# Kernel optimization log

Hardware: AMD Instinct MI355X
Metric: run time of the kernel (lower is better)

Reference implementation:

```python
import jax, jax.numpy as jnp
import numpy as np

EMBED_DIM = 64
N_EMBED = 1024
BATCH, H, W = 16, 64, 64


def setup_inputs() -> dict:
    key = jax.random.key(0)
    k1, k2 = jax.random.split(key)
    inputs = jax.random.normal(k1, (BATCH, H, W, EMBED_DIM), dtype=jnp.float32)
    # codebook as in Quantize.build: RandomNormal(stddev=1.0), shape (embed_dim, n_embed)
    cluster_mean = jax.random.normal(k2, (EMBED_DIM, N_EMBED), dtype=jnp.float32)
    return {"inputs": inputs, "cluster_mean": cluster_mean}


def reference(inputs, cluster_mean):
    # inputs: [B,H,W,D]; cluster_mean: [D,K]
    D = cluster_mean.shape[0]
    samples = inputs.reshape(-1, D)  # [N,D]
    dist = (
        jnp.sum(samples * samples, axis=1, keepdims=True)
        - 2.0 * (samples @ cluster_mean)
        + jnp.sum(cluster_mean * cluster_mean, axis=0, keepdims=True)
    )
    cluster_index = jnp.argmin(dist, axis=1).reshape(inputs.shape[:-1])  # [B,H,W]
    quantize = cluster_mean.T[cluster_index]  # gather -> [B,H,W,D]
    q_loss = jnp.mean((quantize - jax.lax.stop_gradient(inputs)) ** 2)
    e_loss = jnp.mean((jax.lax.stop_gradient(quantize) - inputs) ** 2)
    loss = q_loss + 0.25 * e_loss
    # straight-through estimator
    outputs = inputs + jax.lax.stop_gradient(quantize - inputs)
    return outputs, cluster_index, loss
```

## Files before the change

### kernel.cpp

```cpp
#include <hip/hip_runtime.h>
#include <stdint.h>

#define NS 65536
#define D 64
#define K 1024
#define NEL 4194304
#define MARGIN_KEY 0.025f

typedef short bf16x8 __attribute__((ext_vector_type(8)));
typedef short s16x4 __attribute__((ext_vector_type(4)));
typedef float f32x4 __attribute__((ext_vector_type(4)));

static __device__ __forceinline__ unsigned short bf16_rne(float x) {
    union { float f; uint32_t u; } v; v.f = x;
    uint32_t r = v.u + 0x7FFFu + ((v.u >> 16) & 1u);
    return (unsigned short)(r >> 16);
}
static __device__ __forceinline__ float bf16f(unsigned short h) {
    union { uint32_t u; float f; } v; v.u = ((uint32_t)h) << 16;
    return v.f;
}

__global__ __launch_bounds__(256) void vq_prep(
    const float* __restrict__ cm,
    unsigned short* __restrict__ P,
    float* __restrict__ cnorm,
    double* __restrict__ acc)
{
    const int tx = threadIdx.x;
    const int col = tx & 15;
    const int dg = tx >> 4;
    const int b = blockIdx.x;
    const int k = b * 16 + col;
    if (b == 0 && tx == 0) *acc = 0.0;

    float p = 0.f;
    s16x4 hv, lv;
#pragma unroll
    for (int j = 0; j < 4; ++j) {
        float v = cm[(dg * 4 + j) * K + k];
        unsigned short hb = bf16_rne(v);
        hv[j] = (short)hb;
        lv[j] = (short)bf16_rne(v - bf16f(hb));
        p = fmaf(v, v, p);
    }
    const int lane = ((dg >> 1) & 3) * 16 + col;
    const int e0 = (dg & 1) * 4;
    unsigned short* ph = P + ((size_t)(b * 4 + (dg >> 3)) * 64 + lane) * 8 + e0;
    unsigned short* pl = P + ((size_t)(b * 4 + 2 + (dg >> 3)) * 64 + lane) * 8 + e0;
    *(s16x4*)ph = hv;
    *(s16x4*)pl = lv;

    __shared__ float pn[16][17];
    pn[col][dg] = p;
    __syncthreads();
    if (tx < 16) {
        float s = 0.f;
#pragma unroll
        for (int g = 0; g < 16; ++g) s += pn[tx][g];
        cnorm[b * 16 + tx] = s;
    }
}

__global__ __launch_bounds__(256, 2) void vq_main(
    const float* __restrict__ xin,
    const float* __restrict__ cm,
    const unsigned short* __restrict__ P,
    const float* __restrict__ cnorm,
    float* __restrict__ outq,
    float* __restrict__ outidx,
    double* __restrict__ acc_g)
{
    __shared__ char smemA[36864];
    __shared__ unsigned short btile[4][2048];
    __shared__ float cn_lds[1024];
    __shared__ int   widx[128];

    unsigned short* xh = (unsigned short*)smemA;
    unsigned short* xl = (unsigned short*)(smemA + 18432);
    float* mb1 = (float*)smemA;
    float* mb2 = (float*)(smemA + 8704);
    float* red = (float*)smemA;

    const int tx = threadIdx.x;
    const int S0 = blockIdx.x * 128;
    const int w = tx >> 6, l = tx & 63;
    const int quad = l >> 4, col = l & 15;

#define ISSUE(T) do {                                                          \
        const unsigned short* g_ = P + (size_t)(T) * 2048 + tx * 8;            \
        __builtin_amdgcn_global_load_lds(g_, &btile[(T) & 3][tx * 8], 16, 0, 0); \
    } while (0)
#define WAITV(N) asm volatile("s_waitcnt vmcnt(" #N ")" ::: "memory")

    ISSUE(0); ISSUE(1); ISSUE(2);

    {
        const int s = tx >> 2, d0 = (tx & 3) * 16;
#pragma unroll
        for (int half = 0; half < 2; ++half) {
            const int ss = s + half * 64;
            const float* gp = xin + (size_t)(S0 + ss) * D + d0;
            bf16x8 hv0, hv1, lv0, lv1;
#pragma unroll
            for (int j = 0; j < 8; ++j) {
                float va = -gp[j], vb = -gp[8 + j];
                unsigned short ha = bf16_rne(va), hb = bf16_rne(vb);
                hv0[j] = (short)ha; hv1[j] = (short)hb;
                lv0[j] = (short)bf16_rne(va - bf16f(ha));
                lv1[j] = (short)bf16_rne(vb - bf16f(hb));
            }
            *(bf16x8*)(xh + ss * 72 + d0)     = hv0;
            *(bf16x8*)(xh + ss * 72 + d0 + 8) = hv1;
            *(bf16x8*)(xl + ss * 72 + d0)     = lv0;
            *(bf16x8*)(xl + ss * 72 + d0 + 8) = lv1;
        }
#pragma unroll
        for (int q = 0; q < 4; ++q)
            cn_lds[q * 256 + tx] = 0.5f * cnorm[q * 256 + tx];
    }
    __syncthreads();

    bf16x8 AH0[2], AH1[2], AL0[2], AL1[2];
#pragma unroll
    for (int sg = 0; sg < 2; ++sg) {
        const int srow = w * 32 + sg * 16 + col;
        AH0[sg] = *(const bf16x8*)(xh + srow * 72 + quad * 8);
        AH1[sg] = *(const bf16x8*)(xh + srow * 72 + 32 + quad * 8);
        AL0[sg] = *(const bf16x8*)(xl + srow * 72 + quad * 8);
        AL1[sg] = *(const bf16x8*)(xl + srow * 72 + 32 + quad * 8);
    }

    float b1[2][4], b2[2][4];
#pragma unroll
    for (int sg = 0; sg < 2; ++sg)
#pragma unroll
        for (int r = 0; r < 4; ++r) { b1[sg][r] = 3.4e38f; b2[sg][r] = 3.4e38f; }

#define BODY(T) do {                                                           \
        const unsigned short* bt_ = &btile[(T) & 3][0];                        \
        bf16x8 bh0 = *(const bf16x8*)(bt_ + l * 8);                            \
        bf16x8 bh1 = *(const bf16x8*)(bt_ + 512 + l * 8);                      \
        bf16x8 bl0 = *(const bf16x8*)(bt_ + 1024 + l * 8);                     \
        bf16x8 bl1 = *(const bf16x8*)(bt_ + 1536 + l * 8);                     \
        const float cnv_ = cn_lds[(T) * 16 + col];                             \
        const f32x4 cA_ = {cnv_, cnv_, cnv_, cnv_};                            \
        const f32x4 z4_ = {0.f, 0.f, 0.f, 0.f};                                \
        const unsigned tt_ = (unsigned)(T);                                    \
        _Pragma("unroll")                                                      \
        for (int sg = 0; sg < 2; ++sg) {                                       \
            f32x4 a1_ = __builtin_amdgcn_mfma_f32_16x16x32_bf16(AH0[sg], bh0, cA_, 0, 0, 0); \
            a1_ = __builtin_amdgcn_mfma_f32_16x16x32_bf16(AH1[sg], bh1, a1_, 0, 0, 0); \
            a1_ = __builtin_amdgcn_mfma_f32_16x16x32_bf16(AL0[sg], bh0, a1_, 0, 0, 0); \
            f32x4 a2_ = __builtin_amdgcn_mfma_f32_16x16x32_bf16(AH0[sg], bl0, z4_, 0, 0, 0); \
            a2_ = __builtin_amdgcn_mfma_f32_16x16x32_bf16(AH1[sg], bl1, a2_, 0, 0, 0); \
            a2_ = __builtin_amdgcn_mfma_f32_16x16x32_bf16(AL1[sg], bh1, a2_, 0, 0, 0); \
            _Pragma("unroll")                                                  \
            for (int r = 0; r < 4; ++r) {                                      \
                float v_ = a1_[r] + a2_[r];                                    \
                unsigned pu_ = (__builtin_bit_cast(unsigned, v_) & 0xFFFFFFC0u) | tt_; \
                float f_ = __builtin_bit_cast(float, pu_);                     \
                b2[sg][r] = __builtin_amdgcn_fmed3f(b1[sg][r], f_, b2[sg][r]); \
                b1[sg][r] = fminf(b1[sg][r], f_);                              \
            }                                                                  \
        }                                                                      \
    } while (0)

    for (int t = 0; t < 61; ++t) {
        WAITV(2);
        __builtin_amdgcn_s_barrier();
        ISSUE(t + 3);
        BODY(t);
    }
    WAITV(2); __builtin_amdgcn_s_barrier(); BODY(61);
    WAITV(1); __builtin_amdgcn_s_barrier(); BODY(62);
    WAITV(0); __builtin_amdgcn_s_barrier(); BODY(63);

#pragma unroll
    for (int sg = 0; sg < 2; ++sg) {
        const int u = (w * 2 + sg) * 64 + l;
        const int sk = 4 * (u + (u >> 4));
#pragma unroll
        for (int r = 0; r < 4; ++r) {
            mb1[sk + r] = b1[sg][r];
            mb2[sk + r] = b2[sg][r];
        }
    }
    __syncthreads();

    if (tx < 128) {
        const int mw = tx >> 5, msg = (tx >> 4) & 1, mq = (tx >> 2) & 3, mr = tx & 3;
        float B1 = 3.4e38f, B2 = 3.4e38f; int I1 = 0, I2 = 0;
#pragma unroll
        for (int c = 0; c < 16; ++c) {
            const int u = (mw * 2 + msg) * 64 + mq * 16 + c;
            const int e = 4 * (u + (u >> 4)) + mr;
            float v1 = mb1[e];
            float v2 = mb2[e];
            int j1 = (int)(__builtin_bit_cast(unsigned, v1) & 63u) * 16 + c;
            int j2 = (int)(__builtin_bit_cast(unsigned, v2) & 63u) * 16 + c;
            if (v1 < B1)      { B2 = B1; I2 = I1; B1 = v1; I1 = j1; }
            else if (v1 < B2) { B2 = v1; I2 = j1; }
            if (v2 < B1)      { B2 = B1; I2 = I1; B1 = v2; I1 = j2; }
            else if (v2 < B2) { B2 = v2; I2 = j2; }
        }
        int winner = I1;
        if (B2 - B1 < MARGIN_KEY) {
            const float* xp = xin + (size_t)(S0 + tx) * D;
            float a0 = 0, a1 = 0, a2 = 0, a3 = 0, e0 = 0, e1 = 0, e2 = 0, e3 = 0;
            for (int dd = 0; dd < D; dd += 4) {
                float x0 = xp[dd], x1 = xp[dd + 1], x2 = xp[dd + 2], x3 = xp[dd + 3];
                a0 = fmaf(x0, cm[(dd + 0) * K + I1], a0);
                a1 = fmaf(x1, cm[(dd + 1) * K + I1], a1);
                a2 = fmaf(x2, cm[(dd + 2) * K + I1], a2);
                a3 = fmaf(x3, cm[(dd + 3) * K + I1], a3);
                e0 = fmaf(x0, cm[(dd + 0) * K + I2], e0);
                e1 = fmaf(x1, cm[(dd + 1) * K + I2], e1);
                e2 = fmaf(x2, cm[(dd + 2) * K + I2], e2);
                e3 = fmaf(x3, cm[(dd + 3) * K + I2], e3);
            }
            float d1 = cn_lds[I1] - ((a0 + a1) + (a2 + a3));
            float d2 = cn_lds[I2] - ((e0 + e1) + (e2 + e3));
            if (d2 < d1 || (d2 == d1 && I2 < I1)) winner = I2;
        }
        widx[tx] = winner;
    }
    __syncthreads();

    float psum = 0.f;
#pragma unroll
    for (int half = 0; half < 2; ++half) {
        const int sl = (tx >> 2) + half * 64, d0 = (tx & 3) * 16;
        const int gs = S0 + sl;
        const int wi = widx[sl];
        const int gt = wi >> 4, gc = wi & 15;
        const int qq = (d0 >> 3) & 3;
        const int gf = d0 >> 5;
        const unsigned short* gh = P + ((size_t)((gt * 4 + gf) * 64) + qq * 16 + gc) * 8;
        const unsigned short* gl = P + ((size_t)((gt * 4 + 2 + gf) * 64) + qq * 16 + gc) * 8;
        bf16x8 h0 = *(const bf16x8*)(gh);
        bf16x8 h1 = *(const bf16x8*)(gh + 128);
        bf16x8 l0 = *(const bf16x8*)(gl);
        bf16x8 l1 = *(const bf16x8*)(gl + 128);
        const float* xr = xin + (size_t)gs * D + d0;
        float* oq = outq + (size_t)gs * D + d0;
#pragma unroll
        for (int g = 0; g < 4; ++g) {
            float4 xv = *(const float4*)(xr + 4 * g);
            float q0 = bf16f((unsigned short)(g < 2 ? h0[4 * g + 0] : h1[4 * g - 8 + 0])) +
                       bf16f((unsigned short)(g < 2 ? l0[4 * g + 0] : l1[4 * g - 8 + 0]));
            float q1 = bf16f((unsigned short)(g < 2 ? h0[4 * g + 1] : h1[4 * g - 8 + 1])) +
                       bf16f((unsigned short)(g < 2 ? l0[4 * g + 1] : l1[4 * g - 8 + 1]));
            float q2 = bf16f((unsigned short)(g < 2 ? h0[4 * g + 2] : h1[4 * g - 8 + 2])) +
                       bf16f((unsigned short)(g < 2 ? l0[4 * g + 2] : l1[4 * g - 8 + 2]));
            float q3 = bf16f((unsigned short)(g < 2 ? h0[4 * g + 3] : h1[4 * g - 8 + 3])) +
                       bf16f((unsigned short)(g < 2 ? l0[4 * g + 3] : l1[4 * g - 8 + 3]));
            float dx = q0 - xv.x, dy = q1 - xv.y, dz = q2 - xv.z, dw = q3 - xv.w;
            float4 o;
            o.x = xv.x + dx; o.y = xv.y + dy; o.z = xv.z + dz; o.w = xv.w + dw;
            *(float4*)(oq + 4 * g) = o;
            psum = fmaf(dx, dx, psum);
            psum = fmaf(dy, dy, psum);
            psum = fmaf(dz, dz, psum);
            psum = fmaf(dw, dw, psum);
        }
    }

    if (tx < 128)
        outidx[S0 + tx] = (float)widx[tx];

    __syncthreads();
    red[tx] = psum;
    __syncthreads();
    for (int st = 128; st > 0; st >>= 1) {
        if (tx < st) red[tx] += red[tx + st];
        __syncthreads();
    }
    if (tx == 0) atomicAdd(acc_g, (double)red[0]);
#undef ISSUE
#undef WAITV
#undef BODY
}

__global__ void vq_finalize(const double* __restrict__ acc,
                            float* __restrict__ loss_out)
{
    float m = (float)(*acc / (double)NEL);
    *loss_out = m + 0.25f * m;
}

extern "C" void kernel_launch(void* const* d_in, const int* in_sizes, int n_in,
                              void* d_out, int out_size, void* d_ws, size_t ws_size,
                              hipStream_t stream) {
    const float* xin = (const float*)d_in[0];
    const float* cm  = (const float*)d_in[1];

    float* out     = (float*)d_out;
    float* outq    = out;
    float* outidx  = out + NEL;
    float* outloss = out + NEL + NS;

    unsigned short* P = (unsigned short*)d_ws;
    float*  cnorm = (float*)((char*)d_ws + 262144);
    double* acc   = (double*)((char*)d_ws + 266240);

    vq_prep<<<64, 256, 0, stream>>>(cm, P, cnorm, acc);
    vq_main<<<512, 256, 0, stream>>>(xin, cm, P, cnorm, outq, outidx, acc);
    vq_finalize<<<1, 1, 0, stream>>>(acc, outloss);
}
```

Baseline: 123.1 us.

## Switch distance GEMM to 32x32x16 MFMA and fold loss finalize into main kernel

The distance computation moves from 16x16x32 bf16 MFMA tiles to 32x32x16 tiles over 32 codewords per step. The codebook workspace layout, prep kernel, LDS ring and top-2 merge are reorganised to match, and the main loop shrinks from 64 to 32 iterations. The input is no longer negated; the half-norm is now subtracted from the accumulator after the MFMA chain instead of seeding it. The separate finalize launch is replaced by a last-block-done atomic counter inside the main kernel, trading one launch for a fence and atomic per block. Each thread now holds 16 accumulator values plus 16 entries each of the two running minima, which raises register pressure.

```diff
diff --git a/kernel.cpp b/kernel.cpp
--- a/kernel.cpp
+++ b/kernel.cpp
@@ -8,8 +8,8 @@
 #define MARGIN_KEY 0.025f
 
 typedef short bf16x8 __attribute__((ext_vector_type(8)));
-typedef short s16x4 __attribute__((ext_vector_type(4)));
 typedef float f32x4 __attribute__((ext_vector_type(4)));
+typedef float f32x16 __attribute__((ext_vector_type(16)));
 
 static __device__ __forceinline__ unsigned short bf16_rne(float x) {
     union { float f; uint32_t u; } v; v.f = x;
@@ -25,40 +25,38 @@
     const float* __restrict__ cm,
     unsigned short* __restrict__ P,
     float* __restrict__ cnorm,
-    double* __restrict__ acc)
+    double* __restrict__ acc,
+    unsigned int* __restrict__ cnt)
 {
     const int tx = threadIdx.x;
-    const int col = tx & 15;
-    const int dg = tx >> 4;
-    const int b = blockIdx.x;
-    const int k = b * 16 + col;
-    if (b == 0 && tx == 0) *acc = 0.0;
+    const int c  = tx & 31;
+    const int dg = tx >> 5;
+    const int t  = blockIdx.x;
+    const int k  = t * 32 + c;
+    if (t == 0 && tx == 0) { *acc = 0.0; *cnt = 0u; }
 
     float p = 0.f;
-    s16x4 hv, lv;
-#pragma unroll
-    for (int j = 0; j < 4; ++j) {
-        float v = cm[(dg * 4 + j) * K + k];
+    bf16x8 hv, lv;
+#pragma unroll
+    for (int j = 0; j < 8; ++j) {
+        float v = cm[(dg * 8 + j) * K + k];
         unsigned short hb = bf16_rne(v);
         hv[j] = (short)hb;
         lv[j] = (short)bf16_rne(v - bf16f(hb));
         p = fmaf(v, v, p);
     }
-    const int lane = ((dg >> 1) & 3) * 16 + col;
-    const int e0 = (dg & 1) * 4;
-    unsigned short* ph = P + ((size_t)(b * 4 + (dg >> 3)) * 64 + lane) * 8 + e0;
-    unsigned short* pl = P + ((size_t)(b * 4 + 2 + (dg >> 3)) * 64 + lane) * 8 + e0;
-    *(s16x4*)ph = hv;
-    *(s16x4*)pl = lv;
-
-    __shared__ float pn[16][17];
-    pn[col][dg] = p;
-    __syncthreads();
-    if (tx < 16) {
-        float s = 0.f;
-#pragma unroll
-        for (int g = 0; g < 16; ++g) s += pn[tx][g];
-        cnorm[b * 16 + tx] = s;
+    const int s = dg >> 1, kh = dg & 1;
+    *(bf16x8*)(P + ((size_t)(t * 8 + s) * 64 + kh * 32 + c) * 8)     = hv;
+    *(bf16x8*)(P + ((size_t)(t * 8 + 4 + s) * 64 + kh * 32 + c) * 8) = lv;
+
+    __shared__ float pn[32][9];
+    pn[c][dg] = p;
+    __syncthreads();
+    if (tx < 32) {
+        float sm = 0.f;
+#pragma unroll
+        for (int g = 0; g < 8; ++g) sm += pn[tx][g];
+        cnorm[t * 32 + tx] = sm;
     }
 }
 
@@ -69,51 +67,52 @@
     const float* __restrict__ cnorm,
     float* __restrict__ outq,
     float* __restrict__ outidx,
-    double* __restrict__ acc_g)
+    double* __restrict__ acc_g,
+    unsigned int* __restrict__ cnt_g,
+    float* __restrict__ loss_out)
 {
     __shared__ char smemA[36864];
-    __shared__ unsigned short btile[4][2048];
+    __shared__ unsigned short ring[4][4096];
     __shared__ float cn_lds[1024];
     __shared__ int   widx[128];
 
     unsigned short* xh = (unsigned short*)smemA;
     unsigned short* xl = (unsigned short*)(smemA + 18432);
     float* mb1 = (float*)smemA;
-    float* mb2 = (float*)(smemA + 8704);
+    float* mb2 = (float*)(smemA + 16896);
     float* red = (float*)smemA;
 
     const int tx = threadIdx.x;
     const int S0 = blockIdx.x * 128;
     const int w = tx >> 6, l = tx & 63;
-    const int quad = l >> 4, col = l & 15;
 
 #define ISSUE(T) do {                                                          \
-        const unsigned short* g_ = P + (size_t)(T) * 2048 + tx * 8;            \
-        __builtin_amdgcn_global_load_lds(g_, &btile[(T) & 3][tx * 8], 16, 0, 0); \
+        const unsigned short* g_ = P + (size_t)(T) * 4096 + tx * 8;            \
+        __builtin_amdgcn_global_load_lds(g_, &ring[(T) & 3][tx * 8], 16, 0, 0);\
+        __builtin_amdgcn_global_load_lds(g_ + 2048, &ring[(T) & 3][2048 + tx * 8], 16, 0, 0); \
     } while (0)
 #define WAITV(N) asm volatile("s_waitcnt vmcnt(" #N ")" ::: "memory")
 
     ISSUE(0); ISSUE(1); ISSUE(2);
 
     {
-        const int s = tx >> 2, d0 = (tx & 3) * 16;
-#pragma unroll
-        for (int half = 0; half < 2; ++half) {
-            const int ss = s + half * 64;
-            const float* gp = xin + (size_t)(S0 + ss) * D + d0;
+        const int sr = tx >> 1, dh = (tx & 1) * 32;
+        const float* gp = xin + (size_t)(S0 + sr) * D + dh;
+#pragma unroll
+        for (int g = 0; g < 2; ++g) {
             bf16x8 hv0, hv1, lv0, lv1;
 #pragma unroll
             for (int j = 0; j < 8; ++j) {
-                float va = -gp[j], vb = -gp[8 + j];
+                float va = gp[g * 16 + j], vb = gp[g * 16 + 8 + j];
                 unsigned short ha = bf16_rne(va), hb = bf16_rne(vb);
                 hv0[j] = (short)ha; hv1[j] = (short)hb;
                 lv0[j] = (short)bf16_rne(va - bf16f(ha));
                 lv1[j] = (short)bf16_rne(vb - bf16f(hb));
             }
-            *(bf16x8*)(xh + ss * 72 + d0)     = hv0;
-            *(bf16x8*)(xh + ss * 72 + d0 + 8) = hv1;
-            *(bf16x8*)(xl + ss * 72 + d0)     = lv0;
-            *(bf16x8*)(xl + ss * 72 + d0 + 8) = lv1;
+            *(bf16x8*)(xh + sr * 72 + dh + g * 16)     = hv0;
+            *(bf16x8*)(xh + sr * 72 + dh + g * 16 + 8) = hv1;
+            *(bf16x8*)(xl + sr * 72 + dh + g * 16)     = lv0;
+            *(bf16x8*)(xl + sr * 72 + dh + g * 16 + 8) = lv1;
         }
 #pragma unroll
         for (int q = 0; q < 4; ++q)
@@ -121,84 +120,89 @@
     }
     __syncthreads();
 
-    bf16x8 AH0[2], AH1[2], AL0[2], AL1[2];
-#pragma unroll
-    for (int sg = 0; sg < 2; ++sg) {
-        const int srow = w * 32 + sg * 16 + col;
-        AH0[sg] = *(const bf16x8*)(xh + srow * 72 + quad * 8);
-        AH1[sg] = *(const bf16x8*)(xh + srow * 72 + 32 + quad * 8);
-        AL0[sg] = *(const bf16x8*)(xl + srow * 72 + quad * 8);
-        AL1[sg] = *(const bf16x8*)(xl + srow * 72 + 32 + quad * 8);
-    }
-
-    float b1[2][4], b2[2][4];
-#pragma unroll
-    for (int sg = 0; sg < 2; ++sg)
-#pragma unroll
-        for (int r = 0; r < 4; ++r) { b1[sg][r] = 3.4e38f; b2[sg][r] = 3.4e38f; }
+    const int arow = w * 32 + (l & 31);
+    const int kh8 = (l >> 5) * 8;
+    bf16x8 AH0 = *(const bf16x8*)(xh + arow * 72 + 0  + kh8);
+    bf16x8 AH1 = *(const bf16x8*)(xh + arow * 72 + 16 + kh8);
+    bf16x8 AH2 = *(const bf16x8*)(xh + arow * 72 + 32 + kh8);
+    bf16x8 AH3 = *(const bf16x8*)(xh + arow * 72 + 48 + kh8);
+    bf16x8 AL0 = *(const bf16x8*)(xl + arow * 72 + 0  + kh8);
+    bf16x8 AL1 = *(const bf16x8*)(xl + arow * 72 + 16 + kh8);
+    bf16x8 AL2 = *(const bf16x8*)(xl + arow * 72 + 32 + kh8);
+    bf16x8 AL3 = *(const bf16x8*)(xl + arow * 72 + 48 + kh8);
+
+    float b1[16], b2[16];
+#pragma unroll
+    for (int j = 0; j < 16; ++j) { b1[j] = 3.4e38f; b2[j] = 3.4e38f; }
+
+    const f32x16 Z16 = {0.f,0.f,0.f,0.f,0.f,0.f,0.f,0.f,
+                        0.f,0.f,0.f,0.f,0.f,0.f,0.f,0.f};
 
 #define BODY(T) do {                                                           \
-        const unsigned short* bt_ = &btile[(T) & 3][0];                        \
-        bf16x8 bh0 = *(const bf16x8*)(bt_ + l * 8);                            \
-        bf16x8 bh1 = *(const bf16x8*)(bt_ + 512 + l * 8);                      \
-        bf16x8 bl0 = *(const bf16x8*)(bt_ + 1024 + l * 8);                     \
-        bf16x8 bl1 = *(const bf16x8*)(bt_ + 1536 + l * 8);                     \
-        const float cnv_ = cn_lds[(T) * 16 + col];                             \
-        const f32x4 cA_ = {cnv_, cnv_, cnv_, cnv_};                            \
-        const f32x4 z4_ = {0.f, 0.f, 0.f, 0.f};                                \
+        const unsigned short* bt_ = &ring[(T) & 3][0];                         \
+        bf16x8 Bh0 = *(const bf16x8*)(bt_ + 0    + l * 8);                     \
+        bf16x8 Bh1 = *(const bf16x8*)(bt_ + 512  + l * 8);                     \
+        bf16x8 Bh2 = *(const bf16x8*)(bt_ + 1024 + l * 8);                     \
+        bf16x8 Bh3 = *(const bf16x8*)(bt_ + 1536 + l * 8);                     \
+        bf16x8 Bl0 = *(const bf16x8*)(bt_ + 2048 + l * 8);                     \
+        bf16x8 Bl1 = *(const bf16x8*)(bt_ + 2560 + l * 8);                     \
+        bf16x8 Bl2 = *(const bf16x8*)(bt_ + 3072 + l * 8);                     \
+        bf16x8 Bl3 = *(const bf16x8*)(bt_ + 3584 + l * 8);                     \
+        f32x16 a_ = Z16;                                                       \
+        a_ = __builtin_amdgcn_mfma_f32_32x32x16_bf16(AH0, Bh0, a_, 0, 0, 0);   \
+        a_ = __builtin_amdgcn_mfma_f32_32x32x16_bf16(AH1, Bh1, a_, 0, 0, 0);   \
+        a_ = __builtin_amdgcn_mfma_f32_32x32x16_bf16(AH2, Bh2, a_, 0, 0, 0);   \
+        a_ = __builtin_amdgcn_mfma_f32_32x32x16_bf16(AH3, Bh3, a_, 0, 0, 0);   \
+        a_ = __builtin_amdgcn_mfma_f32_32x32x16_bf16(AH0, Bl0, a_, 0, 0, 0);   \
+        a_ = __builtin_amdgcn_mfma_f32_32x32x16_bf16(AH1, Bl1, a_, 0, 0, 0);   \
+        a_ = __builtin_amdgcn_mfma_f32_32x32x16_bf16(AH2, Bl2, a_, 0, 0, 0);   \
+        a_ = __builtin_amdgcn_mfma_f32_32x32x16_bf16(AH3, Bl3, a_, 0, 0, 0);   \
+        a_ = __builtin_amdgcn_mfma_f32_32x32x16_bf16(AL0, Bh0, a_, 0, 0, 0);   \
+        a_ = __builtin_amdgcn_mfma_f32_32x32x16_bf16(AL1, Bh1, a_, 0, 0, 0);   \
+        a_ = __builtin_amdgcn_mfma_f32_32x32x16_bf16(AL2, Bh2, a_, 0, 0, 0);   \
+        a_ = __builtin_amdgcn_mfma_f32_32x32x16_bf16(AL3, Bh3, a_, 0, 0, 0);   \
+        const float ch_ = cn_lds[(T) * 32 + (l & 31)];                         \
         const unsigned tt_ = (unsigned)(T);                                    \
         _Pragma("unroll")                                                      \
-        for (int sg = 0; sg < 2; ++sg) {                                       \
-            f32x4 a1_ = __builtin_amdgcn_mfma_f32_16x16x32_bf16(AH0[sg], bh0, cA_, 0, 0, 0); \
-            a1_ = __builtin_amdgcn_mfma_f32_16x16x32_bf16(AH1[sg], bh1, a1_, 0, 0, 0); \
-            a1_ = __builtin_amdgcn_mfma_f32_16x16x32_bf16(AL0[sg], bh0, a1_, 0, 0, 0); \
-            f32x4 a2_ = __builtin_amdgcn_mfma_f32_16x16x32_bf16(AH0[sg], bl0, z4_, 0, 0, 0); \
-            a2_ = __builtin_amdgcn_mfma_f32_16x16x32_bf16(AH1[sg], bl1, a2_, 0, 0, 0); \
-            a2_ = __builtin_amdgcn_mfma_f32_16x16x32_bf16(AL1[sg], bh1, a2_, 0, 0, 0); \
-            _Pragma("unroll")                                                  \
-            for (int r = 0; r < 4; ++r) {                                      \
-                float v_ = a1_[r] + a2_[r];                                    \
-                unsigned pu_ = (__builtin_bit_cast(unsigned, v_) & 0xFFFFFFC0u) | tt_; \
-                float f_ = __builtin_bit_cast(float, pu_);                     \
-                b2[sg][r] = __builtin_amdgcn_fmed3f(b1[sg][r], f_, b2[sg][r]); \
-                b1[sg][r] = fminf(b1[sg][r], f_);                              \
-            }                                                                  \
+        for (int j = 0; j < 16; ++j) {                                         \
+            float k_ = ch_ - a_[j];                                            \
+            unsigned pu_ = (__builtin_bit_cast(unsigned, k_) & 0xFFFFFFC0u) | tt_; \
+            float f_ = __builtin_bit_cast(float, pu_);                         \
+            b2[j] = __builtin_amdgcn_fmed3f(b1[j], f_, b2[j]);                 \
+            b1[j] = fminf(b1[j], f_);                                          \
         }                                                                      \
     } while (0)
 
-    for (int t = 0; t < 61; ++t) {
-        WAITV(2);
+    for (int t = 0; t < 29; ++t) {
+        WAITV(4);
         __builtin_amdgcn_s_barrier();
         ISSUE(t + 3);
         BODY(t);
     }
-    WAITV(2); __builtin_amdgcn_s_barrier(); BODY(61);
-    WAITV(1); __builtin_amdgcn_s_barrier(); BODY(62);
-    WAITV(0); __builtin_amdgcn_s_barrier(); BODY(63);
-
-#pragma unroll
-    for (int sg = 0; sg < 2; ++sg) {
-        const int u = (w * 2 + sg) * 64 + l;
-        const int sk = 4 * (u + (u >> 4));
-#pragma unroll
-        for (int r = 0; r < 4; ++r) {
-            mb1[sk + r] = b1[sg][r];
-            mb2[sk + r] = b2[sg][r];
+    WAITV(4); __builtin_amdgcn_s_barrier(); BODY(29);
+    WAITV(2); __builtin_amdgcn_s_barrier(); BODY(30);
+    WAITV(0); __builtin_amdgcn_s_barrier(); BODY(31);
+
+    {
+        const int cc = l & 31, hh = l >> 5;
+#pragma unroll
+        for (int j = 0; j < 16; ++j) {
+            const int r = (j & 3) + 8 * (j >> 2) + 4 * hh;
+            const int sr2 = w * 32 + r;
+            mb1[sr2 * 33 + cc] = b1[j];
+            mb2[sr2 * 33 + cc] = b2[j];
         }
     }
     __syncthreads();
 
     if (tx < 128) {
-        const int mw = tx >> 5, msg = (tx >> 4) & 1, mq = (tx >> 2) & 3, mr = tx & 3;
         float B1 = 3.4e38f, B2 = 3.4e38f; int I1 = 0, I2 = 0;
 #pragma unroll
-        for (int c = 0; c < 16; ++c) {
-            const int u = (mw * 2 + msg) * 64 + mq * 16 + c;
-            const int e = 4 * (u + (u >> 4)) + mr;
-            float v1 = mb1[e];
-            float v2 = mb2[e];
-            int j1 = (int)(__builtin_bit_cast(unsigned, v1) & 63u) * 16 + c;
-            int j2 = (int)(__builtin_bit_cast(unsigned, v2) & 63u) * 16 + c;
+        for (int c = 0; c < 32; ++c) {
+            float v1 = mb1[tx * 33 + c];
+            float v2 = mb2[tx * 33 + c];
+            int j1 = (int)(__builtin_bit_cast(unsigned, v1) & 63u) * 32 + c;
+            int j2 = (int)(__builtin_bit_cast(unsigned, v2) & 63u) * 32 + c;
             if (v1 < B1)      { B2 = B1; I2 = I1; B1 = v1; I1 = j1; }
             else if (v1 < B2) { B2 = v1; I2 = j1; }
             if (v2 < B1)      { B2 = B1; I2 = I1; B1 = v2; I1 = j2; }
@@ -233,15 +237,14 @@
         const int sl = (tx >> 2) + half * 64, d0 = (tx & 3) * 16;
         const int gs = S0 + sl;
         const int wi = widx[sl];
-        const int gt = wi >> 4, gc = wi & 15;
-        const int qq = (d0 >> 3) & 3;
-        const int gf = d0 >> 5;
-        const unsigned short* gh = P + ((size_t)((gt * 4 + gf) * 64) + qq * 16 + gc) * 8;
-        const unsigned short* gl = P + ((size_t)((gt * 4 + 2 + gf) * 64) + qq * 16 + gc) * 8;
+        const int gt = wi >> 5, gc = wi & 31;
+        const int s4 = d0 >> 4;
+        const unsigned short* gh = P + ((size_t)(gt * 8 + s4) * 64 + gc) * 8;
+        const unsigned short* gl = P + ((size_t)(gt * 8 + 4 + s4) * 64 + gc) * 8;
         bf16x8 h0 = *(const bf16x8*)(gh);
-        bf16x8 h1 = *(const bf16x8*)(gh + 128);
+        bf16x8 h1 = *(const bf16x8*)(gh + 256);
         bf16x8 l0 = *(const bf16x8*)(gl);
-        bf16x8 l1 = *(const bf16x8*)(gl + 128);
+        bf16x8 l1 = *(const bf16x8*)(gl + 256);
         const float* xr = xin + (size_t)gs * D + d0;
         float* oq = outq + (size_t)gs * D + d0;
 #pragma unroll
@@ -276,17 +279,20 @@
         if (tx < st) red[tx] += red[tx + st];
         __syncthreads();
     }
-    if (tx == 0) atomicAdd(acc_g, (double)red[0]);
+    if (tx == 0) {
+        atomicAdd(acc_g, (double)red[0]);
+        __threadfence();
+        unsigned prev = atomicAdd(cnt_g, 1u);
+        if (prev == gridDim.x - 1) {
+            __threadfence();
+            double a = atomicAdd(acc_g, 0.0);
+            float m = (float)(a / (double)NEL);
+            *loss_out = m + 0.25f * m;
+        }
+    }
 #undef ISSUE
 #undef WAITV
 #undef BODY
-}
-
-__global__ void vq_finalize(const double* __restrict__ acc,
-                            float* __restrict__ loss_out)
-{
-    float m = (float)(*acc / (double)NEL);
-    *loss_out = m + 0.25f * m;
 }
 
 extern "C" void kernel_launch(void* const* d_in, const int* in_sizes, int n_in,
@@ -303,8 +309,9 @@
     unsigned short* P = (unsigned short*)d_ws;
     float*  cnorm = (float*)((char*)d_ws + 262144);
     double* acc   = (double*)((char*)d_ws + 266240);
-
-    vq_prep<<<64, 256, 0, stream>>>(cm, P, cnorm, acc);
-    vq_main<<<512, 256, 0, stream>>>(xin, cm, P, cnorm, outq, outidx, acc);
-    vq_finalize<<<1, 1, 0, stream>>>(acc, outloss);
-}
+    unsigned int* cnt = (unsigned int*)((char*)d_ws + 266248);
+
+    vq_prep<<<32, 256, 0, stream>>>(cm, P, cnorm, acc, cnt);
+    vq_main<<<512, 256, 0, stream>>>(xin, cm, P, cnorm, outq, outidx,
+                                     acc, cnt, outloss);
+}
```

New measurement: 132.5 us. 1.08x slower.
